# Performance work log

Hardware: AMD Instinct MI355X
Metric: run time of the kernel (lower is better)

Reference implementation:

```python
import jax, jax.numpy as jnp
import numpy as np

B, N, K = 32, 64, 128          # batch, atoms per cell, channel width (128x0e + 128x1o)
R_MAX = 5.0
NUM_BESSEL = 8
P_CUT = 5                       # num_polynomial_cutoff
AVG_NEIGH = 16.0                # avg_num_neighbors
H_MLP = 512                     # hidden_dimensions_size, n_hidden_dimensions = 2
FEAT = 5 * K                    # ((num_interactions-1)*4 + 1) * 128 = 640


def silu(x):
    return x * jax.nn.sigmoid(x)


def _bessel_cutoff(r, mask):
    # Bessel radial basis * polynomial cutoff (MACE), masked on valid edges.
    n = jnp.arange(1, NUM_BESSEL + 1, dtype=r.dtype)
    rb = jnp.sqrt(2.0 / R_MAX) * jnp.sin(n * (jnp.pi / R_MAX) * r[..., None]) / r[..., None]
    u = r / R_MAX
    p = float(P_CUT)
    fc = 1.0 - 0.5 * (p + 1) * (p + 2) * u**P_CUT + p * (p + 2) * u**(P_CUT + 1) - 0.5 * p * (p + 1) * u**(P_CUT + 2)
    fc = fc * (u < 1.0)
    return rb * (fc * mask)[..., None]


def _sph(uvec):
    # Real spherical harmonics l=0,1,2 (component normalization), uvec: unit edge vectors.
    x, y, z = uvec[..., 0], uvec[..., 1], uvec[..., 2]
    s3, s5, s15 = 3.0**0.5, 5.0**0.5, 15.0**0.5
    Y0 = jnp.ones_like(x)[..., None]
    Y1 = jnp.stack([s3 * x, s3 * y, s3 * z], -1)
    Y2 = jnp.stack([s15 * x * y, s15 * y * z, 0.5 * s5 * (3 * z * z - 1.0),
                    s15 * x * z, 0.5 * s15 * (x * x - y * y)], -1)
    return Y0, Y1, Y2


def _radial_mlp(x, w0, b0, w1, b1, w2, b2, w3, b3):
    h = silu(x @ w0 + b0)
    h = silu(h @ w1 + b1)
    h = silu(h @ w2 + b2)
    return h @ w3 + b3


def setup_inputs() -> dict:
    key = jax.random.key(0)
    ks = jax.random.split(key, 32)
    f32 = jnp.float32

    def lin(k, fan_in, shape):
        return (jax.random.normal(k, shape, dtype=f32) / np.sqrt(fan_in)).astype(f32)

    inp = {
        "noisy_relative_positions": jax.random.uniform(ks[0], (B, N, 3), dtype=f32),
        "time": jax.random.uniform(ks[1], (B, 1), dtype=f32),
        "unit_cell": (11.0 * jnp.eye(3, dtype=f32) + 0.3 * jax.random.uniform(ks[2], (B, 3, 3), dtype=f32)),
        "w_embed": lin(ks[3], 1, (K,)),
        # interaction 1 radial MLP: 8 -> 64 -> 64 -> 64 -> 3*K (weights for l=0,1,2 paths)
        "r1_w0": lin(ks[4], NUM_BESSEL, (NUM_BESSEL, 64)), "r1_b0": jnp.zeros((64,), f32),
        "r1_w1": lin(ks[5], 64, (64, 64)), "r1_b1": jnp.zeros((64,), f32),
        "r1_w2": lin(ks[6], 64, (64, 64)), "r1_b2": jnp.zeros((64,), f32),
        "r1_w3": lin(ks[7], 64, (64, 3 * K)), "r1_b3": jnp.zeros((3 * K,), f32),
        "mix1_l0": lin(ks[8], K, (K, K)),
        "mix1_l1": lin(ks[9], K, (K, K)),
        "mix1_l2": lin(ks[10], K, (K, K)),
        # interaction 2 radial MLP: 8 -> 64 -> 64 -> 64 -> 2*K (paths 0e x 0e -> 0e, 1o x 1o -> 0e)
        "r2_w0": lin(ks[11], NUM_BESSEL, (NUM_BESSEL, 64)), "r2_b0": jnp.zeros((64,), f32),
        "r2_w1": lin(ks[12], 64, (64, 64)), "r2_b1": jnp.zeros((64,), f32),
        "r2_w2": lin(ks[13], 64, (64, 64)), "r2_b2": jnp.zeros((64,), f32),
        "r2_w3": lin(ks[14], 64, (64, 2 * K)), "r2_b3": jnp.zeros((2 * K,), f32),
        "mix2": lin(ks[15], K, (K, K)),
        # readout MLP: 641 -> 512 -> 512 -> 3
        "mlp_w0": lin(ks[16], FEAT + 1, (FEAT + 1, H_MLP)), "mlp_b0": jnp.zeros((H_MLP,), f32),
        "mlp_w1": lin(ks[17], H_MLP, (H_MLP, H_MLP)), "mlp_b1": jnp.zeros((H_MLP,), f32),
        "mlp_w2": lin(ks[18], H_MLP, (H_MLP, 3)), "mlp_b2": jnp.zeros((3,), f32),
    }
    return inp


def reference(noisy_relative_positions, time, unit_cell, w_embed,
              r1_w0, r1_b0, r1_w1, r1_b1, r1_w2, r1_b2, r1_w3, r1_b3,
              mix1_l0, mix1_l1, mix1_l2,
              r2_w0, r2_b0, r2_w1, r2_b1, r2_w2, r2_b2, r2_w3, r2_b3, mix2,
              mlp_w0, mlp_b0, mlp_w1, mlp_b1, mlp_w2, mlp_b2):
    frac = noisy_relative_positions                      # [B,N,3] fractional
    d = frac[:, :, None, :] - frac[:, None, :, :]        # [B,N,N,3]
    d = d - jnp.round(d)                                 # minimum-image PBC
    dc = jnp.einsum('bijc,bcd->bijd', d, unit_cell)      # cartesian displacements
    r = jnp.sqrt(jnp.maximum(jnp.sum(dc * dc, -1), 1e-12))
    mask = (r < R_MAX) & (~jnp.eye(N, dtype=bool))[None]
    r_safe = jnp.where(mask, r, 1.0)
    uvec = dc / r_safe[..., None] * mask[..., None]      # unit edge vectors (0 off-edge)

    rad = _bessel_cutoff(r_safe, mask)                   # [B,N,N,8]
    Y0, Y1, Y2 = _sph(uvec)                              # [B,N,N,1|3|5]

    h0 = jnp.broadcast_to(w_embed, (B, N, K))            # element embedding (single species)

    # ---- interaction 1: radial-weighted tensor product h_j (x) Y_l, scatter over j ----
    we = _radial_mlp(rad, r1_w0, r1_b0, r1_w1, r1_b1, r1_w2, r1_b2, r1_w3, r1_b3)
    we = we.reshape(B, N, N, 3, K) * mask[..., None, None]
    hj = h0[:, None, :, :]                               # sender features [B,1,N,K]
    msg0 = jnp.einsum('bijk,bijm->bimk', we[..., 0, :] * hj, Y0)[:, :, 0] / AVG_NEIGH  # [B,N,K]
    msg1 = jnp.einsum('bijk,bijm->bimk', we[..., 1, :] * hj, Y1) / AVG_NEIGH           # [B,N,3,K]
    msg2 = jnp.einsum('bijk,bijm->bimk', we[..., 2, :] * hj, Y2) / AVG_NEIGH           # [B,N,5,K]

    s1 = msg0 @ mix1_l0 + jnp.sum(msg2 * msg2, axis=2) @ mix1_l2   # scalars [B,N,K]
    v1 = jnp.einsum('bimk,kc->bimc', msg1, mix1_l1)                # vectors [B,N,3,K]
    h1 = silu(s1)

    # ---- interaction 2: scalar output from 0e x 0e and 1o x 1o -> 0e paths ----
    we2 = _radial_mlp(rad, r2_w0, r2_b0, r2_w1, r2_b1, r2_w2, r2_b2, r2_w3, r2_b3)
    we2 = we2.reshape(B, N, N, 2, K) * mask[..., None, None]
    msg_a = jnp.sum(we2[..., 0, :] * h1[:, None, :, :], axis=2)    # [B,N,K]
    inv = jnp.einsum('bijm,bjmk->bijk', Y1, v1)                    # Y1 . v1_j invariant
    msg_b = jnp.sum(we2[..., 1, :] * inv, axis=2)
    s2 = ((msg_a + msg_b) / AVG_NEIGH) @ mix2                      # [B,N,K]

    # node_feats: layer1 full irreps (128x0e + 128x1o -> 512) + layer2 scalars (128) = 640
    node_feats = jnp.concatenate([s1, v1.reshape(B, N, 3 * K), s2], axis=-1)

    t = jnp.broadcast_to(time[:, None, :], (B, N, 1))
    x = jnp.concatenate([node_feats, t], axis=-1)                  # [B,N,641]
    x = jax.nn.relu(x @ mlp_w0 + mlp_b0)
    x = jax.nn.relu(x @ mlp_w1 + mlp_b1)
    return x @ mlp_w2 + mlp_b2                                     # [B,N,3]
```

## Files before the change

kernel.cpp:

```cpp
#include <hip/hip_runtime.h>
#include <math.h>

#define B_ 32
#define N_ 64
#define K_ 128
#define NPAIR (B_*N_*N_)

typedef __attribute__((ext_vector_type(8))) short short8;
typedef __attribute__((ext_vector_type(8))) __bf16 bf16x8;
typedef __attribute__((ext_vector_type(4))) float floatx4;

__device__ __forceinline__ float silu_f(float x) {
    return x / (1.0f + expf(-x));
}
__device__ __forceinline__ float4 ld4(const float* p) { return *(const float4*)p; }

__device__ __forceinline__ short f2bf(float x) {
    union { float f; unsigned u; } v; v.f = x;
    unsigned r = (v.u + 0x7FFFu + ((v.u >> 16) & 1u)) >> 16;
    return (short)r;
}
__device__ __forceinline__ float bf2f(short s) {
    union { unsigned u; float f; } v;
    v.u = ((unsigned)(unsigned short)s) << 16;
    return v.f;
}
__device__ __forceinline__ bf16x8 ld_frag(const short* p) {
    short8 r = *(const short8*)p;
    return __builtin_bit_cast(bf16x8, r);
}

__global__ __launch_bounds__(256) void prep_kernel(
    const float* __restrict__ r1w0, const float* __restrict__ r1w1,
    const float* __restrict__ r1w2, const float* __restrict__ r1w3,
    const float* __restrict__ r2w0, const float* __restrict__ r2w1,
    const float* __restrict__ r2w2, const float* __restrict__ r2w3,
    const float* __restrict__ mw0, const float* __restrict__ mw1,
    const float* __restrict__ wemb,
    const float* __restrict__ l0, const float* __restrict__ l1,
    const float* __restrict__ l2, short* __restrict__ dst)
{
    int idx = blockIdx.x * 256 + threadIdx.x;
    if (idx >= 733184) return;
    short v;
    if (idx < 4096) {
        int n = idx >> 6, k = idx & 63; v = f2bf(r1w1[k*64 + n]);
    } else if (idx < 8192) {
        int i = idx - 4096; int n = i >> 6, k = i & 63; v = f2bf(r1w2[k*64 + n]);
    } else if (idx < 12288) {
        int i = idx - 8192; int n = i >> 6, k = i & 63; v = f2bf(r2w1[k*64 + n]);
    } else if (idx < 16384) {
        int i = idx - 12288; int n = i >> 6, k = i & 63; v = f2bf(r2w2[k*64 + n]);
    } else if (idx < 32768) {
        int i = idx - 16384; int col = i >> 6, h = i & 63; v = f2bf(r2w3[h*256 + col]);
    } else if (idx < 393216) {
        int i = idx - 32768; int n = i / 704, k = i - n*704;
        v = (k < 641) ? f2bf(mw0[(size_t)k*512 + n]) : (short)0;
    } else if (idx < 655360) {
        int i = idx - 393216; int n = i >> 9, k = i & 511;
        v = f2bf(mw1[(size_t)k*512 + n]);
    } else if (idx < 657408) {
        int i = idx - 655360; int n = i >> 5, k = i & 31;
        v = (k < 8) ? f2bf(r1w0[k*64 + n]) : (short)0;
    } else if (idx < 659456) {
        int i = idx - 657408; int n = i >> 5, k = i & 31;
        v = (k < 8) ? f2bf(r2w0[k*64 + n]) : (short)0;
    } else if (idx < 684032) {
        int i = idx - 659456; int col = i >> 6, h = i & 63;
        v = f2bf(r1w3[h*384 + col] * wemb[col & 127] * 0.0625f);
    } else {
        int i = idx - 684032; int n = i / 384, k = i - n*384;
        float f;
        if (k < 128)       f = l0[k*128 + n];
        else if (k < 256)  f = l2[(k-128)*128 + n];
        else               f = l1[(k-256)*128 + n];
        v = f2bf(f);
    }
    dst[idx] = v;
}

__global__ __launch_bounds__(256) void geom_kernel(
    const float* __restrict__ pos, const float* __restrict__ cell,
    float* __restrict__ rad, float* __restrict__ Y1, float* __restrict__ Y2,
    float* __restrict__ maskf)
{
    int p = blockIdx.x * 256 + threadIdx.x;
    if (p >= NPAIR) return;
    int b = p >> 12;
    int ij = p & 4095;
    int i = ij >> 6, j = ij & 63;
    const float* pi = pos + (size_t)(b*N_ + i)*3;
    const float* pj = pos + (size_t)(b*N_ + j)*3;
    float d0 = pi[0]-pj[0], d1 = pi[1]-pj[1], d2 = pi[2]-pj[2];
    d0 -= rintf(d0); d1 -= rintf(d1); d2 -= rintf(d2);
    const float* C = cell + b*9;
    float dc0 = d0*C[0] + d1*C[3] + d2*C[6];
    float dc1 = d0*C[1] + d1*C[4] + d2*C[7];
    float dc2 = d0*C[2] + d1*C[5] + d2*C[8];
    float r2 = fmaxf(dc0*dc0 + dc1*dc1 + dc2*dc2, 1e-12f);
    float r = sqrtf(r2);
    bool m = (r < 5.0f) && (i != j);
    float mf = m ? 1.0f : 0.0f;
    float rs = m ? r : 1.0f;
    float inv_rs = 1.0f / rs;
    float x = dc0*inv_rs*mf, y = dc1*inv_rs*mf, z = dc2*inv_rs*mf;
    float u = r * 0.2f;
    float u2 = u*u, u4 = u2*u2, u5 = u4*u;
    float fc = 1.0f - 21.0f*u5 + 35.0f*u5*u - 15.0f*u5*u2;
    fc = (u < 1.0f) ? fc : 0.0f;
    float pref = 0.6324555320336759f * inv_rs * (fc * mf);
    float w = 0.6283185307179586f * rs;
    float sw = sinf(w), cw = cosf(w);
    float c2 = 2.0f * cw;
    float rr[8];
    float sp = 0.f, s = sw;
    #pragma unroll
    for (int n = 0; n < 8; n++) {
        rr[n] = pref * s;
        float ns = c2*s - sp;
        sp = s; s = ns;
    }
    float4 v0 = {rr[0], rr[1], rr[2], rr[3]};
    float4 v1 = {rr[4], rr[5], rr[6], rr[7]};
    *(float4*)&rad[(size_t)p*8]     = v0;
    *(float4*)&rad[(size_t)p*8 + 4] = v1;
    const float s3  = 1.7320508075688772f;
    const float s5  = 2.23606797749979f;
    const float s15 = 3.872983346207417f;
    float* y1 = Y1 + (size_t)p*3;
    y1[0] = s3*x; y1[1] = s3*y; y1[2] = s3*z;
    float* y2 = Y2 + (size_t)p*5;
    y2[0] = s15*x*y;
    y2[1] = s15*y*z;
    y2[2] = 0.5f*s5*(3.0f*z*z - 1.0f);
    y2[3] = s15*x*z;
    y2[4] = 0.5f*s15*(x*x - y*y);
    maskf[p] = mf;
}

template<bool TRANSPOSE_OUT>
__device__ __forceinline__ void mfma_layer_t(
    const short* __restrict__ src, const short* __restrict__ WT,
    const float* __restrict__ bias, short* __restrict__ dst,
    int wv, int qd, int nn)
{
    floatx4 acc[4];
    #pragma unroll
    for (int tt = 0; tt < 4; tt++) acc[tt] = (floatx4){0.f, 0.f, 0.f, 0.f};
    #pragma unroll
    for (int ks = 0; ks < 64; ks += 32) {
        bf16x8 a = ld_frag(&src[(wv*16 + nn)*72 + ks + qd*8]);
        #pragma unroll
        for (int tt = 0; tt < 4; tt++) {
            bf16x8 b = ld_frag(&WT[(tt*16 + nn)*64 + ks + qd*8]);
            acc[tt] = __builtin_amdgcn_mfma_f32_16x16x32_bf16(a, b, acc[tt], 0, 0, 0);
        }
    }
    #pragma unroll
    for (int tt = 0; tt < 4; tt++) {
        int col = tt*16 + nn;
        float bv = bias[col];
        #pragma unroll
        for (int i = 0; i < 4; i++) {
            int row = wv*16 + qd*4 + i;
            short val = f2bf(silu_f(acc[tt][i] + bv));
            if (TRANSPOSE_OUT) dst[col*72 + row] = val;
            else               dst[row*72 + col] = val;
        }
    }
}

__device__ __forceinline__ void mfma_layer0(
    const short* __restrict__ radB, const short* __restrict__ w0T,
    const float* __restrict__ bias, short* __restrict__ dst,
    int wv, int qd, int nn)
{
    bf16x8 a = ld_frag(&radB[(wv*16 + nn)*40 + qd*8]);
    #pragma unroll
    for (int tt = 0; tt < 4; tt++) {
        floatx4 acc = (floatx4){0.f, 0.f, 0.f, 0.f};
        bf16x8 b = ld_frag(&w0T[(tt*16 + nn)*32 + qd*8]);
        acc = __builtin_amdgcn_mfma_f32_16x16x32_bf16(a, b, acc, 0, 0, 0);
        int col = tt*16 + nn;
        float bv = bias[col];
        #pragma unroll
        for (int i = 0; i < 4; i++) {
            int row = wv*16 + qd*4 + i;
            dst[row*72 + col] = f2bf(silu_f(acc[i] + bv));
        }
    }
}

__global__ __launch_bounds__(256) void pass1_kernel(
    const float* __restrict__ rad, const float* __restrict__ Y1g,
    const float* __restrict__ Y2g, const float* __restrict__ maskg,
    const float* __restrict__ wemb,
    const short* __restrict__ w0T, const float* __restrict__ b0,
    const short* __restrict__ w1T, const float* __restrict__ b1,
    const short* __restrict__ w2T, const float* __restrict__ b2,
    const short* __restrict__ w3T, const float* __restrict__ b3,
    const short* __restrict__ lT, const float* __restrict__ timeg,
    float* __restrict__ h1g, float* __restrict__ v1g, short* __restrict__ featsb)
{
    __shared__ __align__(16) char pool[32832];
    short* radB = (short*)pool;
    short* hcT  = (short*)pool;
    short* actA = (short*)(pool + 9216);
    short* actB = (short*)(pool + 18432);
    short* A2   = (short*)(pool + 9216);
    float* msgF = (float*)(pool + 21760);
    short* YmB  = (short*)(pool + 27648);
    short* GB   = (short*)(pool + 29952);
    float* qF   = (float*)(pool + 32256);
    float* SY   = (float*)(pool + 32768);

    int t = threadIdx.x;
    int wv = t >> 6, lane = t & 63, qd = lane >> 4, nn = lane & 15;
    int node = blockIdx.x;
    int b = node >> 6;
    size_t pbase = (size_t)node * 64;

    for (int idx = t; idx < 2560; idx += 256) {
        int j = idx / 40, c = idx - j*40;
        radB[idx] = (c < 8) ? f2bf(rad[pbase*8 + j*8 + c]) : (short)0;
    }
    for (int idx = t; idx < 1152; idx += 256) YmB[idx] = 0;
    __syncthreads();

    if (t < 64) {
        int j = t;
        float mf = maskg[pbase + j];
        YmB[j] = f2bf(mf);
        #pragma unroll
        for (int m = 0; m < 3; m++) YmB[(1+m)*72 + j] = f2bf(Y1g[(pbase+j)*3 + m] * mf);
        #pragma unroll
        for (int m = 0; m < 5; m++) YmB[(4+m)*72 + j] = f2bf(Y2g[(pbase+j)*5 + m] * mf);
    }
    mfma_layer0(radB, w0T, b0, actA, wv, qd, nn);
    __syncthreads();

    mfma_layer_t<false>(actA, w1T, b1, actB, wv, qd, nn);
    __syncthreads();
    mfma_layer_t<true >(actB, w2T, b2, hcT,  wv, qd, nn);
    __syncthreads();

    if (t < 16) {
        float acc = 0.f;
        if (t < 9) for (int j = 0; j < 64; j++) acc += bf2f(YmB[t*72 + j]);
        SY[t] = acc;
    }
    {
        floatx4 accG = (floatx4){0.f, 0.f, 0.f, 0.f};
        #pragma unroll
        for (int ks = 0; ks < 64; ks += 32) {
            bf16x8 a = ld_frag(&YmB[nn*72 + ks + qd*8]);
            bf16x8 bfr = ld_frag(&hcT[(wv*16 + nn)*72 + ks + qd*8]);
            accG = __builtin_amdgcn_mfma_f32_16x16x32_bf16(a, bfr, accG, 0, 0, 0);
        }
        #pragma unroll
        for (int i = 0; i < 4; i++)
            GB[(qd*4 + i)*72 + wv*16 + nn] = f2bf(accG[i]);
    }
    __syncthreads();

    {
        bf16x8 a0f = ld_frag(&GB[nn*72 + 0  + qd*8]);
        bf16x8 a1f = ld_frag(&GB[nn*72 + 32 + qd*8]);
        #pragma unroll
        for (int tl = 0; tl < 6; tl++) {
            int col0 = (wv*6 + tl)*16;
            floatx4 acc = (floatx4){0.f, 0.f, 0.f, 0.f};
            bf16x8 b0f = ld_frag(&w3T[(col0 + nn)*64 + 0  + qd*8]);
            bf16x8 b1f = ld_frag(&w3T[(col0 + nn)*64 + 32 + qd*8]);
            acc = __builtin_amdgcn_mfma_f32_16x16x32_bf16(a0f, b0f, acc, 0, 0, 0);
            acc = __builtin_amdgcn_mfma_f32_16x16x32_bf16(a1f, b1f, acc, 0, 0, 0);
            int col = col0 + nn;
            int csec = col >> 7, k = col & 127;
            #pragma unroll
            for (int i = 0; i < 4; i++) {
                int m = qd*4 + i;
                bool valid = (csec == 0) ? (m == 0)
                           : (csec == 1) ? (m >= 1 && m <= 3)
                                         : (m >= 4 && m <= 8);
                if (valid)
                    msgF[m*128 + k] = acc[i] + SY[m]*b3[col]*wemb[k]*0.0625f;
            }
        }
    }
    __syncthreads();

    if (t < 128) {
        float acc = 0.f;
        #pragma unroll
        for (int m = 4; m < 9; m++) { float v = msgF[m*128 + t]; acc += v*v; }
        qF[t] = acc;
    }
    __syncthreads();

    for (int idx = t; idx < 6272; idx += 256) A2[idx] = 0;
    __syncthreads();
    {
        int idx = t;
        A2[idx] = (idx < 128) ? f2bf(msgF[idx]) : f2bf(qF[idx - 128]);
        if (t < 128) {
            #pragma unroll
            for (int m = 1; m <= 3; m++)
                A2[m*392 + 256 + t] = f2bf(msgF[m*128 + t]);
        }
    }
    __syncthreads();

    #pragma unroll
    for (int tt = 0; tt < 2; tt++) {
        int col = (wv*2 + tt)*16 + nn;
        floatx4 acc = (floatx4){0.f, 0.f, 0.f, 0.f};
        #pragma unroll
        for (int ks = 0; ks < 384; ks += 32) {
            bf16x8 a = ld_frag(&A2[nn*392 + ks + qd*8]);
            bf16x8 bfr = ld_frag(&lT[(size_t)col*384 + ks + qd*8]);
            acc = __builtin_amdgcn_mfma_f32_16x16x32_bf16(a, bfr, acc, 0, 0, 0);
        }
        if (qd == 0) {
            float s1 = acc[0];
            featsb[(size_t)node*704 + col] = f2bf(s1);
            h1g[(size_t)node*128 + col] = silu_f(s1);
            #pragma unroll
            for (int i = 1; i < 4; i++) {
                float v = acc[i];
                v1g[(size_t)node*384 + (i-1)*128 + col] = v;
                featsb[(size_t)node*704 + 128 + (i-1)*128 + col] = f2bf(v);
            }
        }
    }
    if (t == 0) featsb[(size_t)node*704 + 640] = f2bf(timeg[b]);
    if (t < 63) featsb[(size_t)node*704 + 641 + t] = 0;
}

__global__ __launch_bounds__(256) void pass2_kernel(
    const float* __restrict__ rad, const float* __restrict__ Y1g,
    const float* __restrict__ maskg,
    const short* __restrict__ w0T, const float* __restrict__ b0,
    const short* __restrict__ w1T, const float* __restrict__ b1,
    const short* __restrict__ w2T, const float* __restrict__ b2,
    const short* __restrict__ w3T, const float* __restrict__ b3,
    const float* __restrict__ mix2,
    const float* __restrict__ h1g, const float* __restrict__ v1g,
    short* __restrict__ featsb)
{
    __shared__ __align__(16) char pool[46848];
    short* radB  = (short*)pool;
    short* hc    = (short*)pool;
    short* actA  = (short*)(pool + 9216);
    short* actB  = (short*)(pool + 18432);
    short* h1B   = (short*)(pool + 9216);
    short* invB  = (short*)(pool + 27648);
    float* Y1s   = (float*)(pool + 45056);
    float* mask_s= (float*)(pool + 46080);
    float* msgab = (float*)(pool + 46336);

    int t = threadIdx.x;
    int wv = t >> 6, lane = t & 63, qd = lane >> 4, nn = lane & 15;
    int node = blockIdx.x;
    int b = node >> 6;
    size_t pbase = (size_t)node * 64;

    for (int idx = t; idx < 2560; idx += 256) {
        int j = idx / 40, c = idx - j*40;
        radB[idx] = (c < 8) ? f2bf(rad[pbase*8 + j*8 + c]) : (short)0;
    }
    if (t < 64) {
        mask_s[t] = maskg[pbase + t];
        #pragma unroll
        for (int m = 0; m < 3; m++) Y1s[t*4 + m] = Y1g[(pbase+t)*3 + m];
    }
    if (t < 128) msgab[t] = 0.f;
    __syncthreads();

    mfma_layer0(radB, w0T, b0, actA, wv, qd, nn);
    __syncthreads();
    mfma_layer_t<false>(actA, w1T, b1, actB, wv, qd, nn);
    __syncthreads();
    mfma_layer_t<false>(actB, w2T, b2, hc, wv, qd, nn);
    __syncthreads();

    for (int idx = t; idx < 2048; idx += 256) {
        int j = idx >> 5, kq = (idx & 31)*4;
        size_t gj = (size_t)b*64 + j;
        float4 hv = ld4(&h1g[gj*128 + kq]);
        h1B[j*136 + kq + 0] = f2bf(hv.x);
        h1B[j*136 + kq + 1] = f2bf(hv.y);
        h1B[j*136 + kq + 2] = f2bf(hv.z);
        h1B[j*136 + kq + 3] = f2bf(hv.w);
        const float* vb = &v1g[gj*384 + kq];
        float4 vx = ld4(vb), vy = ld4(vb + 128), vz = ld4(vb + 256);
        float yx = Y1s[j*4+0], yy = Y1s[j*4+1], yz = Y1s[j*4+2];
        invB[j*136 + kq + 0] = f2bf(yx*vx.x + yy*vy.x + yz*vz.x);
        invB[j*136 + kq + 1] = f2bf(yx*vx.y + yy*vy.y + yz*vz.y);
        invB[j*136 + kq + 2] = f2bf(yx*vx.z + yy*vy.z + yz*vz.z);
        invB[j*136 + kq + 3] = f2bf(yx*vx.w + yy*vy.w + yz*vz.w);
    }
    __syncthreads();

    {
        bf16x8 aA = ld_frag(&hc[(wv*16 + nn)*72 + 0  + qd*8]);
        bf16x8 aB = ld_frag(&hc[(wv*16 + nn)*72 + 32 + qd*8]);
        #pragma unroll
        for (int g = 0; g < 4; g++) {
            #pragma unroll
            for (int tt = 0; tt < 4; tt++) {
                int col0 = g*64 + tt*16;
                floatx4 acc = (floatx4){0.f, 0.f, 0.f, 0.f};
                bf16x8 b0f = ld_frag(&w3T[(col0 + nn)*64 + 0  + qd*8]);
                bf16x8 b1f = ld_frag(&w3T[(col0 + nn)*64 + 32 + qd*8]);
                acc = __builtin_amdgcn_mfma_f32_16x16x32_bf16(aA, b0f, acc, 0, 0, 0);
                acc = __builtin_amdgcn_mfma_f32_16x16x32_bf16(aB, b1f, acc, 0, 0, 0);
                int col = col0 + nn;
                int k = col & 127;
                float bias = b3[col];
                const short* src = (col < 128) ? h1B : invB;
                float p = 0.f;
                #pragma unroll
                for (int i = 0; i < 4; i++) {
                    int j = wv*16 + qd*4 + i;
                    float we = (acc[i] + bias) * mask_s[j];
                    p += we * bf2f(src[j*136 + k]);
                }
                p += __shfl_xor(p, 16);
                p += __shfl_xor(p, 32);
                if (qd == 0) atomicAdd(&msgab[k], p);
            }
        }
    }
    __syncthreads();

    if (t < 128) {
        float acc = 0.f;
        for (int k = 0; k < 128; k++) acc += msgab[k] * mix2[k*128 + t];
        featsb[(size_t)node*704 + 512 + t] = f2bf(acc * 0.0625f);
    }
}

__global__ __launch_bounds__(256) void gemm_mfma_kernel(
    const short* __restrict__ A, int lda,
    const short* __restrict__ BT, int ldb, int K,
    const float* __restrict__ bias, short* __restrict__ Cout, int ldo)
{
    __shared__ short As[64*72];
    __shared__ short Bs[64*72];
    int t = threadIdx.x;
    int wv = t >> 6, lane = t & 63, qd = lane >> 4, nn = lane & 15;
    int m0 = blockIdx.x * 64, n0 = blockIdx.y * 64;
    floatx4 acc[4];
    #pragma unroll
    for (int tt = 0; tt < 4; tt++) acc[tt] = (floatx4){0.f, 0.f, 0.f, 0.f};

    for (int kc = 0; kc < K; kc += 64) {
        for (int s = t; s < 512; s += 256) {
            int j = s >> 3, kk = (s & 7) * 8;
            *(uint4*)&As[j*72 + kk] = *(const uint4*)&A[(size_t)(m0 + j)*lda + kc + kk];
            *(uint4*)&Bs[j*72 + kk] = *(const uint4*)&BT[(size_t)(n0 + j)*ldb + kc + kk];
        }
        __syncthreads();
        #pragma unroll
        for (int ks = 0; ks < 64; ks += 32) {
            bf16x8 a = ld_frag(&As[(wv*16 + nn)*72 + ks + qd*8]);
            #pragma unroll
            for (int tt = 0; tt < 4; tt++) {
                bf16x8 bb = ld_frag(&Bs[(tt*16 + nn)*72 + ks + qd*8]);
                acc[tt] = __builtin_amdgcn_mfma_f32_16x16x32_bf16(a, bb, acc[tt], 0, 0, 0);
            }
        }
        __syncthreads();
    }
    #pragma unroll
    for (int tt = 0; tt < 4; tt++) {
        int n = n0 + tt*16 + nn;
        float bv = bias[n];
        #pragma unroll
        for (int i = 0; i < 4; i++) {
            int m = m0 + wv*16 + qd*4 + i;
            Cout[(size_t)m*ldo + n] = f2bf(fmaxf(acc[tt][i] + bv, 0.f));
        }
    }
}

__global__ __launch_bounds__(64) void final3_kernel(
    const short* __restrict__ H, const float* __restrict__ w2,
    const float* __restrict__ b2, float* __restrict__ out)
{
    int node = blockIdx.x, lane = threadIdx.x;
    float a0 = 0.f, a1 = 0.f, a2 = 0.f;
    #pragma unroll
    for (int r = 0; r < 8; r++) {
        int k = r*64 + lane;
        float h = bf2f(H[(size_t)node*512 + k]);
        a0 += h * w2[k*3 + 0];
        a1 += h * w2[k*3 + 1];
        a2 += h * w2[k*3 + 2];
    }
    #pragma unroll
    for (int off = 32; off > 0; off >>= 1) {
        a0 += __shfl_down(a0, off);
        a1 += __shfl_down(a1, off);
        a2 += __shfl_down(a2, off);
    }
    if (lane == 0) {
        out[(size_t)node*3 + 0] = a0 + b2[0];
        out[(size_t)node*3 + 1] = a1 + b2[1];
        out[(size_t)node*3 + 2] = a2 + b2[2];
    }
}

extern "C" void kernel_launch(void* const* d_in, const int* in_sizes, int n_in,
                              void* d_out, int out_size, void* d_ws, size_t ws_size,
                              hipStream_t stream) {
    const float* pos   = (const float*)d_in[0];
    const float* timeg = (const float*)d_in[1];
    const float* cell  = (const float*)d_in[2];
    const float* wemb  = (const float*)d_in[3];
    const float* r1w0  = (const float*)d_in[4];
    const float* r1b0  = (const float*)d_in[5];
    const float* r1w1  = (const float*)d_in[6];
    const float* r1b1  = (const float*)d_in[7];
    const float* r1w2  = (const float*)d_in[8];
    const float* r1b2  = (const float*)d_in[9];
    const float* r1w3  = (const float*)d_in[10];
    const float* r1b3  = (const float*)d_in[11];
    const float* l0    = (const float*)d_in[12];
    const float* l1    = (const float*)d_in[13];
    const float* l2    = (const float*)d_in[14];
    const float* r2w0  = (const float*)d_in[15];
    const float* r2b0  = (const float*)d_in[16];
    const float* r2w1  = (const float*)d_in[17];
    const float* r2b1  = (const float*)d_in[18];
    const float* r2w2  = (const float*)d_in[19];
    const float* r2b2  = (const float*)d_in[20];
    const float* r2w3  = (const float*)d_in[21];
    const float* r2b3  = (const float*)d_in[22];
    const float* mix2  = (const float*)d_in[23];
    const float* mw0   = (const float*)d_in[24];
    const float* mb0   = (const float*)d_in[25];
    const float* mw1   = (const float*)d_in[26];
    const float* mb1   = (const float*)d_in[27];
    const float* mw2   = (const float*)d_in[28];
    const float* mb2   = (const float*)d_in[29];

    float* ws    = (float*)d_ws;
    float* rad   = ws;
    float* Y1    = rad   + (size_t)NPAIR*8;
    float* Y2    = Y1    + (size_t)NPAIR*3;
    float* maskf = Y2    + (size_t)NPAIR*5;
    float* h1    = maskf + (size_t)NPAIR;
    float* v1    = h1    + (size_t)B_*N_*K_;
    short* featsb = (short*)(v1 + (size_t)B_*N_*3*K_);
    short* prep  = featsb + (size_t)2048*704;
    short* w1T_1 = prep;
    short* w2T_1 = prep + 4096;
    short* w1T_2 = prep + 8192;
    short* w2T_2 = prep + 12288;
    short* w3T_2 = prep + 16384;
    short* wT0   = prep + 32768;
    short* wT1   = prep + 393216;
    short* w0T_1 = prep + 655360;
    short* w0T_2 = prep + 657408;
    short* w3T_1 = prep + 659456;
    short* lT    = prep + 684032;
    short* h0bb = (short*)rad;
    short* h1bb = (short*)Y2;

    prep_kernel<<<(733184 + 255)/256, 256, 0, stream>>>(
        r1w0, r1w1, r1w2, r1w3, r2w0, r2w1, r2w2, r2w3, mw0, mw1,
        wemb, l0, l1, l2, prep);
    geom_kernel<<<NPAIR/256, 256, 0, stream>>>(pos, cell, rad, Y1, Y2, maskf);
    pass1_kernel<<<B_*N_, 256, 0, stream>>>(rad, Y1, Y2, maskf, wemb,
        w0T_1, r1b0, w1T_1, r1b1, w2T_1, r1b2, w3T_1, r1b3, lT, timeg,
        h1, v1, featsb);
    pass2_kernel<<<B_*N_, 256, 0, stream>>>(rad, Y1, maskf,
        w0T_2, r2b0, w1T_2, r2b1, w2T_2, r2b2, w3T_2, r2b3, mix2, h1, v1, featsb);
    dim3 g0(32, 8);
    gemm_mfma_kernel<<<g0, 256, 0, stream>>>(featsb, 704, wT0, 704, 704, mb0, h0bb, 512);
    gemm_mfma_kernel<<<g0, 256, 0, stream>>>(h0bb, 512, wT1, 512, 512, mb1, h1bb, 512);
    final3_kernel<<<B_*N_, 64, 0, stream>>>(h1bb, mw2, mb2, (float*)d_out);
}
```

Measured before the change: 292.2 us.

## Split radial MLPs into batched kernel, split-K head GEMMs, MFMA mix2 projection

The radial MLP hidden layers for both interactions move out of the per-node pass kernels into one bigmlp kernel that processes 128 edges per block and writes bf16 hidden activations to global memory. The message kernels then only run the final projection, and the r2 bias is folded into an extended weight. The radial basis and h1 are now stored as bf16. The mix2 projection moves from a scalar loop to a separate MFMA kernel. The head MLP GEMMs become split-K over 4 partitions with a combine kernel, which adds launches and extra global round trips of hidden and partial data in exchange for more parallelism.

```diff
diff --git a/kernel.cpp b/kernel.cpp
--- a/kernel.cpp
+++ b/kernel.cpp
@@ -35,13 +35,15 @@
     const float* __restrict__ r1w2, const float* __restrict__ r1w3,
     const float* __restrict__ r2w0, const float* __restrict__ r2w1,
     const float* __restrict__ r2w2, const float* __restrict__ r2w3,
+    const float* __restrict__ r2b3,
     const float* __restrict__ mw0, const float* __restrict__ mw1,
     const float* __restrict__ wemb,
     const float* __restrict__ l0, const float* __restrict__ l1,
-    const float* __restrict__ l2, short* __restrict__ dst)
+    const float* __restrict__ l2, const float* __restrict__ mix2,
+    short* __restrict__ dst)
 {
     int idx = blockIdx.x * 256 + threadIdx.x;
-    if (idx >= 733184) return;
+    if (idx >= 757760) return;
     short v;
     if (idx < 4096) {
         int n = idx >> 6, k = idx & 63; v = f2bf(r1w1[k*64 + n]);
@@ -51,37 +53,42 @@
         int i = idx - 8192; int n = i >> 6, k = i & 63; v = f2bf(r2w1[k*64 + n]);
     } else if (idx < 16384) {
         int i = idx - 12288; int n = i >> 6, k = i & 63; v = f2bf(r2w2[k*64 + n]);
-    } else if (idx < 32768) {
-        int i = idx - 16384; int col = i >> 6, h = i & 63; v = f2bf(r2w3[h*256 + col]);
-    } else if (idx < 393216) {
-        int i = idx - 32768; int n = i / 704, k = i - n*704;
+    } else if (idx < 40960) {
+        int i = idx - 16384; int col = i / 96, k = i - col*96;
+        v = (k < 64) ? f2bf(r2w3[k*256 + col])
+          : (k == 64) ? f2bf(r2b3[col]) : (short)0;
+    } else if (idx < 401408) {
+        int i = idx - 40960; int n = i / 704, k = i - n*704;
         v = (k < 641) ? f2bf(mw0[(size_t)k*512 + n]) : (short)0;
-    } else if (idx < 655360) {
-        int i = idx - 393216; int n = i >> 9, k = i & 511;
+    } else if (idx < 663552) {
+        int i = idx - 401408; int n = i >> 9, k = i & 511;
         v = f2bf(mw1[(size_t)k*512 + n]);
-    } else if (idx < 657408) {
-        int i = idx - 655360; int n = i >> 5, k = i & 31;
+    } else if (idx < 665600) {
+        int i = idx - 663552; int n = i >> 5, k = i & 31;
         v = (k < 8) ? f2bf(r1w0[k*64 + n]) : (short)0;
-    } else if (idx < 659456) {
-        int i = idx - 657408; int n = i >> 5, k = i & 31;
+    } else if (idx < 667648) {
+        int i = idx - 665600; int n = i >> 5, k = i & 31;
         v = (k < 8) ? f2bf(r2w0[k*64 + n]) : (short)0;
-    } else if (idx < 684032) {
-        int i = idx - 659456; int col = i >> 6, h = i & 63;
+    } else if (idx < 692224) {
+        int i = idx - 667648; int col = i >> 6, h = i & 63;
         v = f2bf(r1w3[h*384 + col] * wemb[col & 127] * 0.0625f);
-    } else {
-        int i = idx - 684032; int n = i / 384, k = i - n*384;
+    } else if (idx < 741376) {
+        int i = idx - 692224; int n = i / 384, k = i - n*384;
         float f;
         if (k < 128)       f = l0[k*128 + n];
         else if (k < 256)  f = l2[(k-128)*128 + n];
         else               f = l1[(k-256)*128 + n];
         v = f2bf(f);
+    } else {
+        int i = idx - 741376; int n = i >> 7, k = i & 127;
+        v = f2bf(mix2[k*128 + n] * 0.0625f);
     }
     dst[idx] = v;
 }
 
 __global__ __launch_bounds__(256) void geom_kernel(
     const float* __restrict__ pos, const float* __restrict__ cell,
-    float* __restrict__ rad, float* __restrict__ Y1, float* __restrict__ Y2,
+    short* __restrict__ radbf, float* __restrict__ Y1, float* __restrict__ Y2,
     float* __restrict__ maskf)
 {
     int p = blockIdx.x * 256 + threadIdx.x;
@@ -112,18 +119,15 @@
     float w = 0.6283185307179586f * rs;
     float sw = sinf(w), cw = cosf(w);
     float c2 = 2.0f * cw;
-    float rr[8];
+    short8 sv;
     float sp = 0.f, s = sw;
     #pragma unroll
     for (int n = 0; n < 8; n++) {
-        rr[n] = pref * s;
+        sv[n] = f2bf(pref * s);
         float ns = c2*s - sp;
         sp = s; s = ns;
     }
-    float4 v0 = {rr[0], rr[1], rr[2], rr[3]};
-    float4 v1 = {rr[4], rr[5], rr[6], rr[7]};
-    *(float4*)&rad[(size_t)p*8]     = v0;
-    *(float4*)&rad[(size_t)p*8 + 4] = v1;
+    *(short8*)&radbf[(size_t)p*8] = sv;
     const float s3  = 1.7320508075688772f;
     const float s5  = 2.23606797749979f;
     const float s15 = 3.872983346207417f;
@@ -138,81 +142,126 @@
     maskf[p] = mf;
 }
 
-template<bool TRANSPOSE_OUT>
-__device__ __forceinline__ void mfma_layer_t(
-    const short* __restrict__ src, const short* __restrict__ WT,
-    const float* __restrict__ bias, short* __restrict__ dst,
-    int wv, int qd, int nn)
-{
-    floatx4 acc[4];
-    #pragma unroll
-    for (int tt = 0; tt < 4; tt++) acc[tt] = (floatx4){0.f, 0.f, 0.f, 0.f};
-    #pragma unroll
-    for (int ks = 0; ks < 64; ks += 32) {
-        bf16x8 a = ld_frag(&src[(wv*16 + nn)*72 + ks + qd*8]);
-        #pragma unroll
-        for (int tt = 0; tt < 4; tt++) {
-            bf16x8 b = ld_frag(&WT[(tt*16 + nn)*64 + ks + qd*8]);
-            acc[tt] = __builtin_amdgcn_mfma_f32_16x16x32_bf16(a, b, acc[tt], 0, 0, 0);
-        }
-    }
-    #pragma unroll
-    for (int tt = 0; tt < 4; tt++) {
-        int col = tt*16 + nn;
-        float bv = bias[col];
-        #pragma unroll
-        for (int i = 0; i < 4; i++) {
-            int row = wv*16 + qd*4 + i;
-            short val = f2bf(silu_f(acc[tt][i] + bv));
-            if (TRANSPOSE_OUT) dst[col*72 + row] = val;
-            else               dst[row*72 + col] = val;
-        }
-    }
-}
-
-__device__ __forceinline__ void mfma_layer0(
-    const short* __restrict__ radB, const short* __restrict__ w0T,
-    const float* __restrict__ bias, short* __restrict__ dst,
-    int wv, int qd, int nn)
-{
-    bf16x8 a = ld_frag(&radB[(wv*16 + nn)*40 + qd*8]);
-    #pragma unroll
-    for (int tt = 0; tt < 4; tt++) {
-        floatx4 acc = (floatx4){0.f, 0.f, 0.f, 0.f};
-        bf16x8 b = ld_frag(&w0T[(tt*16 + nn)*32 + qd*8]);
-        acc = __builtin_amdgcn_mfma_f32_16x16x32_bf16(a, b, acc, 0, 0, 0);
-        int col = tt*16 + nn;
-        float bv = bias[col];
-        #pragma unroll
-        for (int i = 0; i < 4; i++) {
-            int row = wv*16 + qd*4 + i;
-            dst[row*72 + col] = f2bf(silu_f(acc[i] + bv));
-        }
-    }
-}
-
-__global__ __launch_bounds__(256) void pass1_kernel(
-    const float* __restrict__ rad, const float* __restrict__ Y1g,
+__global__ __launch_bounds__(256) void bigmlp_kernel(
+    const short* __restrict__ radbf,
+    const short* __restrict__ w0T1, const float* __restrict__ b01,
+    const short* __restrict__ w1T1, const float* __restrict__ b11,
+    const short* __restrict__ w2T1, const float* __restrict__ b21,
+    short* __restrict__ hc1,
+    const short* __restrict__ w0T2, const float* __restrict__ b02,
+    const short* __restrict__ w1T2, const float* __restrict__ b12,
+    const short* __restrict__ w2T2, const float* __restrict__ b22,
+    short* __restrict__ hc2)
+{
+    __shared__ short radB[128*40];
+    __shared__ short actA[128*72];
+    __shared__ short actB[128*72];
+    int t = threadIdx.x;
+    int wv = t >> 6, lane = t & 63, qd = lane >> 4, nn = lane & 15;
+    size_t p0 = (size_t)blockIdx.x * 128;
+
+    if (t < 128) {
+        uint4 rv = *(const uint4*)&radbf[(p0 + t)*8];
+        uint4 z = {0,0,0,0};
+        *(uint4*)&radB[t*40]      = rv;
+        *(uint4*)&radB[t*40 + 8]  = z;
+        *(uint4*)&radB[t*40 + 16] = z;
+        *(uint4*)&radB[t*40 + 24] = z;
+        *(uint4*)&radB[t*40 + 32] = z;
+    }
+    __syncthreads();
+
+    const short* w0Ts[2] = {w0T1, w0T2};
+    const short* w1Ts[2] = {w1T1, w1T2};
+    const short* w2Ts[2] = {w2T1, w2T2};
+    const float* b0s[2]  = {b01, b02};
+    const float* b1s[2]  = {b11, b12};
+    const float* b2s[2]  = {b21, b22};
+    short* hcs[2] = {hc1, hc2};
+
+    for (int net = 0; net < 2; net++) {
+        const short* w0T = w0Ts[net];
+        const short* w1T = w1Ts[net];
+        const short* w2T = w2Ts[net];
+        const float* b0 = b0s[net];
+        const float* b1 = b1s[net];
+        const float* b2 = b2s[net];
+        short* hc = hcs[net];
+        #pragma unroll
+        for (int ms = 0; ms < 2; ms++) {
+            int r0 = wv*32 + ms*16;
+            bf16x8 a = ld_frag(&radB[(r0 + nn)*40 + qd*8]);
+            #pragma unroll
+            for (int tt = 0; tt < 4; tt++) {
+                floatx4 acc = (floatx4){0.f,0.f,0.f,0.f};
+                bf16x8 bb = ld_frag(&w0T[(tt*16 + nn)*32 + qd*8]);
+                acc = __builtin_amdgcn_mfma_f32_16x16x32_bf16(a, bb, acc, 0, 0, 0);
+                int col = tt*16 + nn;
+                float bv = b0[col];
+                #pragma unroll
+                for (int i = 0; i < 4; i++)
+                    actA[(r0 + qd*4 + i)*72 + col] = f2bf(silu_f(acc[i] + bv));
+            }
+        }
+        __syncthreads();
+        #pragma unroll
+        for (int ms = 0; ms < 2; ms++) {
+            int r0 = wv*32 + ms*16;
+            bf16x8 a0 = ld_frag(&actA[(r0 + nn)*72 + qd*8]);
+            bf16x8 a1 = ld_frag(&actA[(r0 + nn)*72 + 32 + qd*8]);
+            #pragma unroll
+            for (int tt = 0; tt < 4; tt++) {
+                floatx4 acc = (floatx4){0.f,0.f,0.f,0.f};
+                bf16x8 b0f = ld_frag(&w1T[(tt*16 + nn)*64 + qd*8]);
+                bf16x8 b1f = ld_frag(&w1T[(tt*16 + nn)*64 + 32 + qd*8]);
+                acc = __builtin_amdgcn_mfma_f32_16x16x32_bf16(a0, b0f, acc, 0, 0, 0);
+                acc = __builtin_amdgcn_mfma_f32_16x16x32_bf16(a1, b1f, acc, 0, 0, 0);
+                int col = tt*16 + nn;
+                float bv = b1[col];
+                #pragma unroll
+                for (int i = 0; i < 4; i++)
+                    actB[(r0 + qd*4 + i)*72 + col] = f2bf(silu_f(acc[i] + bv));
+            }
+        }
+        __syncthreads();
+        #pragma unroll
+        for (int ms = 0; ms < 2; ms++) {
+            int r0 = wv*32 + ms*16;
+            bf16x8 a0 = ld_frag(&actB[(r0 + nn)*72 + qd*8]);
+            bf16x8 a1 = ld_frag(&actB[(r0 + nn)*72 + 32 + qd*8]);
+            #pragma unroll
+            for (int tt = 0; tt < 4; tt++) {
+                floatx4 acc = (floatx4){0.f,0.f,0.f,0.f};
+                bf16x8 b0f = ld_frag(&w2T[(tt*16 + nn)*64 + qd*8]);
+                bf16x8 b1f = ld_frag(&w2T[(tt*16 + nn)*64 + 32 + qd*8]);
+                acc = __builtin_amdgcn_mfma_f32_16x16x32_bf16(a0, b0f, acc, 0, 0, 0);
+                acc = __builtin_amdgcn_mfma_f32_16x16x32_bf16(a1, b1f, acc, 0, 0, 0);
+                int col = tt*16 + nn;
+                float bv = b2[col];
+                #pragma unroll
+                for (int i = 0; i < 4; i++)
+                    hc[(p0 + r0 + qd*4 + i)*64 + col] = f2bf(silu_f(acc[i] + bv));
+            }
+        }
+    }
+}
+
+__global__ __launch_bounds__(256) void msg1_kernel(
+    const short* __restrict__ hc1, const float* __restrict__ Y1g,
     const float* __restrict__ Y2g, const float* __restrict__ maskg,
-    const float* __restrict__ wemb,
-    const short* __restrict__ w0T, const float* __restrict__ b0,
-    const short* __restrict__ w1T, const float* __restrict__ b1,
-    const short* __restrict__ w2T, const float* __restrict__ b2,
-    const short* __restrict__ w3T, const float* __restrict__ b3,
-    const short* __restrict__ lT, const float* __restrict__ timeg,
-    float* __restrict__ h1g, float* __restrict__ v1g, short* __restrict__ featsb)
-{
-    __shared__ __align__(16) char pool[32832];
-    short* radB = (short*)pool;
+    const float* __restrict__ wemb, const float* __restrict__ b3,
+    const short* __restrict__ w3T, const short* __restrict__ lT,
+    const float* __restrict__ timeg,
+    short* __restrict__ h1bf, float* __restrict__ v1g, short* __restrict__ featsb)
+{
+    __shared__ __align__(16) char pool[19008];
     short* hcT  = (short*)pool;
-    short* actA = (short*)(pool + 9216);
-    short* actB = (short*)(pool + 18432);
-    short* A2   = (short*)(pool + 9216);
-    float* msgF = (float*)(pool + 21760);
-    short* YmB  = (short*)(pool + 27648);
-    short* GB   = (short*)(pool + 29952);
-    float* qF   = (float*)(pool + 32256);
-    float* SY   = (float*)(pool + 32768);
+    short* A2   = (short*)pool;
+    short* YmB  = (short*)(pool + 9216);
+    short* GB   = (short*)(pool + 11520);
+    float* msgF = (float*)(pool + 13824);
+    float* qF   = (float*)(pool + 18432);
+    float* SY   = (float*)(pool + 18944);
 
     int t = threadIdx.x;
     int wv = t >> 6, lane = t & 63, qd = lane >> 4, nn = lane & 15;
@@ -220,13 +269,14 @@
     int b = node >> 6;
     size_t pbase = (size_t)node * 64;
 
-    for (int idx = t; idx < 2560; idx += 256) {
-        int j = idx / 40, c = idx - j*40;
-        radB[idx] = (c < 8) ? f2bf(rad[pbase*8 + j*8 + c]) : (short)0;
+    for (int idx = t; idx < 512; idx += 256) {
+        int j = idx >> 3, h0 = (idx & 7)*8;
+        short8 v = *(const short8*)&hc1[((size_t)node*64 + j)*64 + h0];
+        #pragma unroll
+        for (int q = 0; q < 8; q++) hcT[(h0 + q)*72 + j] = v[q];
     }
     for (int idx = t; idx < 1152; idx += 256) YmB[idx] = 0;
     __syncthreads();
-
     if (t < 64) {
         int j = t;
         float mf = maskg[pbase + j];
@@ -236,21 +286,14 @@
         #pragma unroll
         for (int m = 0; m < 5; m++) YmB[(4+m)*72 + j] = f2bf(Y2g[(pbase+j)*5 + m] * mf);
     }
-    mfma_layer0(radB, w0T, b0, actA, wv, qd, nn);
-    __syncthreads();
-
-    mfma_layer_t<false>(actA, w1T, b1, actB, wv, qd, nn);
-    __syncthreads();
-    mfma_layer_t<true >(actB, w2T, b2, hcT,  wv, qd, nn);
-    __syncthreads();
-
+    __syncthreads();
     if (t < 16) {
         float acc = 0.f;
         if (t < 9) for (int j = 0; j < 64; j++) acc += bf2f(YmB[t*72 + j]);
         SY[t] = acc;
     }
     {
-        floatx4 accG = (floatx4){0.f, 0.f, 0.f, 0.f};
+        floatx4 accG = (floatx4){0.f,0.f,0.f,0.f};
         #pragma unroll
         for (int ks = 0; ks < 64; ks += 32) {
             bf16x8 a = ld_frag(&YmB[nn*72 + ks + qd*8]);
@@ -262,14 +305,13 @@
             GB[(qd*4 + i)*72 + wv*16 + nn] = f2bf(accG[i]);
     }
     __syncthreads();
-
     {
         bf16x8 a0f = ld_frag(&GB[nn*72 + 0  + qd*8]);
         bf16x8 a1f = ld_frag(&GB[nn*72 + 32 + qd*8]);
         #pragma unroll
         for (int tl = 0; tl < 6; tl++) {
             int col0 = (wv*6 + tl)*16;
-            floatx4 acc = (floatx4){0.f, 0.f, 0.f, 0.f};
+            floatx4 acc = (floatx4){0.f,0.f,0.f,0.f};
             bf16x8 b0f = ld_frag(&w3T[(col0 + nn)*64 + 0  + qd*8]);
             bf16x8 b1f = ld_frag(&w3T[(col0 + nn)*64 + 32 + qd*8]);
             acc = __builtin_amdgcn_mfma_f32_16x16x32_bf16(a0f, b0f, acc, 0, 0, 0);
@@ -288,7 +330,6 @@
         }
     }
     __syncthreads();
-
     if (t < 128) {
         float acc = 0.f;
         #pragma unroll
@@ -296,24 +337,19 @@
         qF[t] = acc;
     }
     __syncthreads();
-
     for (int idx = t; idx < 6272; idx += 256) A2[idx] = 0;
     __syncthreads();
-    {
-        int idx = t;
-        A2[idx] = (idx < 128) ? f2bf(msgF[idx]) : f2bf(qF[idx - 128]);
-        if (t < 128) {
-            #pragma unroll
-            for (int m = 1; m <= 3; m++)
-                A2[m*392 + 256 + t] = f2bf(msgF[m*128 + t]);
-        }
-    }
-    __syncthreads();
-
+    A2[t] = (t < 128) ? f2bf(msgF[t]) : f2bf(qF[t - 128]);
+    if (t < 128) {
+        #pragma unroll
+        for (int m = 1; m <= 3; m++)
+            A2[m*392 + 256 + t] = f2bf(msgF[m*128 + t]);
+    }
+    __syncthreads();
     #pragma unroll
     for (int tt = 0; tt < 2; tt++) {
         int col = (wv*2 + tt)*16 + nn;
-        floatx4 acc = (floatx4){0.f, 0.f, 0.f, 0.f};
+        floatx4 acc = (floatx4){0.f,0.f,0.f,0.f};
         #pragma unroll
         for (int ks = 0; ks < 384; ks += 32) {
             bf16x8 a = ld_frag(&A2[nn*392 + ks + qd*8]);
@@ -323,7 +359,7 @@
         if (qd == 0) {
             float s1 = acc[0];
             featsb[(size_t)node*704 + col] = f2bf(s1);
-            h1g[(size_t)node*128 + col] = silu_f(s1);
+            h1bf[(size_t)node*128 + col] = f2bf(silu_f(s1));
             #pragma unroll
             for (int i = 1; i < 4; i++) {
                 float v = acc[i];
@@ -336,27 +372,18 @@
     if (t < 63) featsb[(size_t)node*704 + 641 + t] = 0;
 }
 
-__global__ __launch_bounds__(256) void pass2_kernel(
-    const float* __restrict__ rad, const float* __restrict__ Y1g,
-    const float* __restrict__ maskg,
-    const short* __restrict__ w0T, const float* __restrict__ b0,
-    const short* __restrict__ w1T, const float* __restrict__ b1,
-    const short* __restrict__ w2T, const float* __restrict__ b2,
-    const short* __restrict__ w3T, const float* __restrict__ b3,
-    const float* __restrict__ mix2,
-    const float* __restrict__ h1g, const float* __restrict__ v1g,
-    short* __restrict__ featsb)
-{
-    __shared__ __align__(16) char pool[46848];
-    short* radB  = (short*)pool;
-    short* hc    = (short*)pool;
-    short* actA  = (short*)(pool + 9216);
-    short* actB  = (short*)(pool + 18432);
-    short* h1B   = (short*)(pool + 9216);
-    short* invB  = (short*)(pool + 27648);
-    float* Y1s   = (float*)(pool + 45056);
-    float* mask_s= (float*)(pool + 46080);
-    float* msgab = (float*)(pool + 46336);
+__global__ __launch_bounds__(256) void msg2_kernel(
+    const short* __restrict__ hc2, const float* __restrict__ Y1g,
+    const float* __restrict__ maskg, const short* __restrict__ w3extT,
+    const short* __restrict__ h1bf, const float* __restrict__ v1g,
+    short* __restrict__ msgabf)
+{
+    __shared__ __align__(16) char pool[50688];
+    short* hc2e  = (short*)pool;
+    short* h1B   = (short*)(pool + 14336);
+    short* invB  = (short*)(pool + 31744);
+    float* Y1s   = (float*)(pool + 49152);
+    float* msgab = (float*)(pool + 50176);
 
     int t = threadIdx.x;
     int wv = t >> 6, lane = t & 63, qd = lane >> 4, nn = lane & 15;
@@ -364,34 +391,36 @@
     int b = node >> 6;
     size_t pbase = (size_t)node * 64;
 
-    for (int idx = t; idx < 2560; idx += 256) {
-        int j = idx / 40, c = idx - j*40;
-        radB[idx] = (c < 8) ? f2bf(rad[pbase*8 + j*8 + c]) : (short)0;
-    }
     if (t < 64) {
-        mask_s[t] = maskg[pbase + t];
-        #pragma unroll
-        for (int m = 0; m < 3; m++) Y1s[t*4 + m] = Y1g[(pbase+t)*3 + m];
+        int j = t;
+        #pragma unroll
+        for (int m = 0; m < 3; m++) Y1s[j*4 + m] = Y1g[(pbase+j)*3 + m];
+        float mf = maskg[pbase + j];
+        short8 z8 = {0,0,0,0,0,0,0,0};
+        *(short8*)&hc2e[j*112 + 64] = z8;
+        *(short8*)&hc2e[j*112 + 72] = z8;
+        *(short8*)&hc2e[j*112 + 80] = z8;
+        *(short8*)&hc2e[j*112 + 88] = z8;
+        *(short8*)&hc2e[j*112 + 96] = z8;
+        *(short8*)&hc2e[j*112 + 104] = z8;
+        hc2e[j*112 + 64] = f2bf(mf);
+    }
+    for (int idx = t; idx < 512; idx += 256) {
+        int j = idx >> 3, h0 = (idx & 7)*8;
+        short8 v = *(const short8*)&hc2[((size_t)node*64 + j)*64 + h0];
+        float mf = maskg[pbase + j];
+        if (mf == 0.f) { short8 z8 = {0,0,0,0,0,0,0,0}; v = z8; }
+        *(short8*)&hc2e[j*112 + h0] = v;
+    }
+    for (int idx = t; idx < 1024; idx += 256) {
+        int j = idx >> 4, k0 = (idx & 15)*8;
+        *(uint4*)&h1B[j*136 + k0] = *(const uint4*)&h1bf[((size_t)b*64 + j)*128 + k0];
     }
     if (t < 128) msgab[t] = 0.f;
     __syncthreads();
-
-    mfma_layer0(radB, w0T, b0, actA, wv, qd, nn);
-    __syncthreads();
-    mfma_layer_t<false>(actA, w1T, b1, actB, wv, qd, nn);
-    __syncthreads();
-    mfma_layer_t<false>(actB, w2T, b2, hc, wv, qd, nn);
-    __syncthreads();
-
     for (int idx = t; idx < 2048; idx += 256) {
         int j = idx >> 5, kq = (idx & 31)*4;
-        size_t gj = (size_t)b*64 + j;
-        float4 hv = ld4(&h1g[gj*128 + kq]);
-        h1B[j*136 + kq + 0] = f2bf(hv.x);
-        h1B[j*136 + kq + 1] = f2bf(hv.y);
-        h1B[j*136 + kq + 2] = f2bf(hv.z);
-        h1B[j*136 + kq + 3] = f2bf(hv.w);
-        const float* vb = &v1g[gj*384 + kq];
+        const float* vb = &v1g[((size_t)b*64 + j)*384 + kq];
         float4 vx = ld4(vb), vy = ld4(vb + 128), vz = ld4(vb + 256);
         float yx = Y1s[j*4+0], yy = Y1s[j*4+1], yz = Y1s[j*4+2];
         invB[j*136 + kq + 0] = f2bf(yx*vx.x + yy*vy.x + yz*vz.x);
@@ -400,30 +429,29 @@
         invB[j*136 + kq + 3] = f2bf(yx*vx.w + yy*vy.w + yz*vz.w);
     }
     __syncthreads();
-
     {
-        bf16x8 aA = ld_frag(&hc[(wv*16 + nn)*72 + 0  + qd*8]);
-        bf16x8 aB = ld_frag(&hc[(wv*16 + nn)*72 + 32 + qd*8]);
-        #pragma unroll
+        bf16x8 a0 = ld_frag(&hc2e[(wv*16 + nn)*112 + 0  + qd*8]);
+        bf16x8 a1 = ld_frag(&hc2e[(wv*16 + nn)*112 + 32 + qd*8]);
+        bf16x8 a2 = ld_frag(&hc2e[(wv*16 + nn)*112 + 64 + qd*8]);
         for (int g = 0; g < 4; g++) {
             #pragma unroll
             for (int tt = 0; tt < 4; tt++) {
                 int col0 = g*64 + tt*16;
-                floatx4 acc = (floatx4){0.f, 0.f, 0.f, 0.f};
-                bf16x8 b0f = ld_frag(&w3T[(col0 + nn)*64 + 0  + qd*8]);
-                bf16x8 b1f = ld_frag(&w3T[(col0 + nn)*64 + 32 + qd*8]);
-                acc = __builtin_amdgcn_mfma_f32_16x16x32_bf16(aA, b0f, acc, 0, 0, 0);
-                acc = __builtin_amdgcn_mfma_f32_16x16x32_bf16(aB, b1f, acc, 0, 0, 0);
+                floatx4 acc = (floatx4){0.f,0.f,0.f,0.f};
+                bf16x8 b0f = ld_frag(&w3extT[(col0 + nn)*96 + 0  + qd*8]);
+                bf16x8 b1f = ld_frag(&w3extT[(col0 + nn)*96 + 32 + qd*8]);
+                bf16x8 b2f = ld_frag(&w3extT[(col0 + nn)*96 + 64 + qd*8]);
+                acc = __builtin_amdgcn_mfma_f32_16x16x32_bf16(a0, b0f, acc, 0, 0, 0);
+                acc = __builtin_amdgcn_mfma_f32_16x16x32_bf16(a1, b1f, acc, 0, 0, 0);
+                acc = __builtin_amdgcn_mfma_f32_16x16x32_bf16(a2, b2f, acc, 0, 0, 0);
                 int col = col0 + nn;
                 int k = col & 127;
-                float bias = b3[col];
                 const short* src = (col < 128) ? h1B : invB;
                 float p = 0.f;
                 #pragma unroll
                 for (int i = 0; i < 4; i++) {
                     int j = wv*16 + qd*4 + i;
-                    float we = (acc[i] + bias) * mask_s[j];
-                    p += we * bf2f(src[j*136 + k]);
+                    p += acc[i] * bf2f(src[j*136 + k]);
                 }
                 p += __shfl_xor(p, 16);
                 p += __shfl_xor(p, 32);
@@ -432,56 +460,89 @@
         }
     }
     __syncthreads();
-
-    if (t < 128) {
-        float acc = 0.f;
-        for (int k = 0; k < 128; k++) acc += msgab[k] * mix2[k*128 + t];
-        featsb[(size_t)node*704 + 512 + t] = f2bf(acc * 0.0625f);
-    }
-}
-
-__global__ __launch_bounds__(256) void gemm_mfma_kernel(
+    if (t < 128) msgabf[(size_t)node*128 + t] = f2bf(msgab[t]);
+}
+
+__global__ __launch_bounds__(64) void s2_kernel(
+    const short* __restrict__ msgabf, const short* __restrict__ mix2T,
+    short* __restrict__ featsb)
+{
+    int lane = threadIdx.x, qd = lane >> 4, nn = lane & 15;
+    int m0 = blockIdx.x * 16, n0 = blockIdx.y * 64;
+    floatx4 acc[4];
+    #pragma unroll
+    for (int tt = 0; tt < 4; tt++) acc[tt] = (floatx4){0.f,0.f,0.f,0.f};
+    #pragma unroll
+    for (int ks = 0; ks < 128; ks += 32) {
+        bf16x8 a = ld_frag(&msgabf[(size_t)(m0 + nn)*128 + ks + qd*8]);
+        #pragma unroll
+        for (int tt = 0; tt < 4; tt++) {
+            bf16x8 bb = ld_frag(&mix2T[(size_t)(n0 + tt*16 + nn)*128 + ks + qd*8]);
+            acc[tt] = __builtin_amdgcn_mfma_f32_16x16x32_bf16(a, bb, acc[tt], 0, 0, 0);
+        }
+    }
+    #pragma unroll
+    for (int tt = 0; tt < 4; tt++) {
+        int n = n0 + tt*16 + nn;
+        #pragma unroll
+        for (int i = 0; i < 4; i++) {
+            int m = m0 + qd*4 + i;
+            featsb[(size_t)m*704 + 512 + n] = f2bf(acc[tt][i]);
+        }
+    }
+}
+
+__global__ __launch_bounds__(256) void gemm_part_kernel(
     const short* __restrict__ A, int lda,
-    const short* __restrict__ BT, int ldb, int K,
-    const float* __restrict__ bias, short* __restrict__ Cout, int ldo)
-{
-    __shared__ short As[64*72];
-    __shared__ short Bs[64*72];
+    const short* __restrict__ BT, int ldb,
+    int ngran, int nsplit, float* __restrict__ Cp)
+{
     int t = threadIdx.x;
     int wv = t >> 6, lane = t & 63, qd = lane >> 4, nn = lane & 15;
-    int m0 = blockIdx.x * 64, n0 = blockIdx.y * 64;
+    int m0 = blockIdx.x * 64, n0 = blockIdx.y * 64, z = blockIdx.z;
+    int g0 = (z*ngran)/nsplit, g1 = ((z+1)*ngran)/nsplit;
     floatx4 acc[4];
     #pragma unroll
-    for (int tt = 0; tt < 4; tt++) acc[tt] = (floatx4){0.f, 0.f, 0.f, 0.f};
-
-    for (int kc = 0; kc < K; kc += 64) {
-        for (int s = t; s < 512; s += 256) {
-            int j = s >> 3, kk = (s & 7) * 8;
-            *(uint4*)&As[j*72 + kk] = *(const uint4*)&A[(size_t)(m0 + j)*lda + kc + kk];
-            *(uint4*)&Bs[j*72 + kk] = *(const uint4*)&BT[(size_t)(n0 + j)*ldb + kc + kk];
-        }
-        __syncthreads();
-        #pragma unroll
-        for (int ks = 0; ks < 64; ks += 32) {
-            bf16x8 a = ld_frag(&As[(wv*16 + nn)*72 + ks + qd*8]);
-            #pragma unroll
-            for (int tt = 0; tt < 4; tt++) {
-                bf16x8 bb = ld_frag(&Bs[(tt*16 + nn)*72 + ks + qd*8]);
-                acc[tt] = __builtin_amdgcn_mfma_f32_16x16x32_bf16(a, bb, acc[tt], 0, 0, 0);
-            }
-        }
-        __syncthreads();
-    }
+    for (int tt = 0; tt < 4; tt++) acc[tt] = (floatx4){0.f,0.f,0.f,0.f};
+    int row = wv*16 + nn;
+    for (int g = g0; g < g1; g++) {
+        int k = g*32;
+        bf16x8 a = ld_frag(&A[(size_t)(m0 + row)*lda + k + qd*8]);
+        #pragma unroll
+        for (int tt = 0; tt < 4; tt++) {
+            bf16x8 bb = ld_frag(&BT[(size_t)(n0 + tt*16 + nn)*ldb + k + qd*8]);
+            acc[tt] = __builtin_amdgcn_mfma_f32_16x16x32_bf16(a, bb, acc[tt], 0, 0, 0);
+        }
+    }
+    float* out = Cp + (size_t)z*2048*512;
     #pragma unroll
     for (int tt = 0; tt < 4; tt++) {
         int n = n0 + tt*16 + nn;
-        float bv = bias[n];
-        #pragma unroll
-        for (int i = 0; i < 4; i++) {
-            int m = m0 + wv*16 + qd*4 + i;
-            Cout[(size_t)m*ldo + n] = f2bf(fmaxf(acc[tt][i] + bv, 0.f));
-        }
-    }
+        #pragma unroll
+        for (int i = 0; i < 4; i++)
+            out[(size_t)(m0 + wv*16 + qd*4 + i)*512 + n] = acc[tt][i];
+    }
+}
+
+__global__ __launch_bounds__(256) void combine_kernel(
+    const float* __restrict__ Cp, const float* __restrict__ bias,
+    short* __restrict__ out)
+{
+    int idx = (blockIdx.x * 256 + threadIdx.x) * 4;
+    int n = idx & 511;
+    float4 s = ld4(&Cp[idx]);
+    #pragma unroll
+    for (int z = 1; z < 4; z++) {
+        float4 p = ld4(&Cp[(size_t)z*1048576 + idx]);
+        s.x += p.x; s.y += p.y; s.z += p.z; s.w += p.w;
+    }
+    float4 bv = ld4(&bias[n]);
+    short4 o;
+    o.x = f2bf(fmaxf(s.x + bv.x, 0.f));
+    o.y = f2bf(fmaxf(s.y + bv.y, 0.f));
+    o.z = f2bf(fmaxf(s.z + bv.z, 0.f));
+    o.w = f2bf(fmaxf(s.w + bv.w, 0.f));
+    *(short4*)&out[idx] = o;
 }
 
 __global__ __launch_bounds__(64) void final3_kernel(
@@ -545,40 +606,57 @@
     const float* mw2   = (const float*)d_in[28];
     const float* mb2   = (const float*)d_in[29];
 
-    float* ws    = (float*)d_ws;
-    float* rad   = ws;
-    float* Y1    = rad   + (size_t)NPAIR*8;
-    float* Y2    = Y1    + (size_t)NPAIR*3;
-    float* maskf = Y2    + (size_t)NPAIR*5;
-    float* h1    = maskf + (size_t)NPAIR;
-    float* v1    = h1    + (size_t)B_*N_*K_;
-    short* featsb = (short*)(v1 + (size_t)B_*N_*3*K_);
-    short* prep  = featsb + (size_t)2048*704;
-    short* w1T_1 = prep;
-    short* w2T_1 = prep + 4096;
-    short* w1T_2 = prep + 8192;
-    short* w2T_2 = prep + 12288;
-    short* w3T_2 = prep + 16384;
-    short* wT0   = prep + 32768;
-    short* wT1   = prep + 393216;
-    short* w0T_1 = prep + 655360;
-    short* w0T_2 = prep + 657408;
-    short* w3T_1 = prep + 659456;
-    short* lT    = prep + 684032;
-    short* h0bb = (short*)rad;
+    float* ws = (float*)d_ws;
+    short* radbf  = (short*)ws;
+    float* Y1     = ws + 524288;
+    float* Y2     = ws + 917504;
+    float* maskf  = ws + 1572864;
+    float* v1     = ws + 1703936;
+    short* featsb = (short*)(ws + 2490368);
+    short* prep   = (short*)(ws + 3211264);
+    short* hc1    = (short*)(ws + 3590144);
+    short* hc2    = (short*)(ws + 7784448);
+    short* h1bf   = (short*)(ws + 11978752);
+    short* msgabf = (short*)(ws + 12109824);
+
+    short* w1T_1  = prep;
+    short* w2T_1  = prep + 4096;
+    short* w1T_2  = prep + 8192;
+    short* w2T_2  = prep + 12288;
+    short* w3extT = prep + 16384;
+    short* wT0    = prep + 40960;
+    short* wT1    = prep + 401408;
+    short* w0T_1  = prep + 663552;
+    short* w0T_2  = prep + 665600;
+    short* w3T_1  = prep + 667648;
+    short* lT     = prep + 692224;
+    short* mix2T  = prep + 741376;
+
+    float* Cp   = (float*)hc1;
+    short* h0bb = radbf;
     short* h1bb = (short*)Y2;
 
-    prep_kernel<<<(733184 + 255)/256, 256, 0, stream>>>(
-        r1w0, r1w1, r1w2, r1w3, r2w0, r2w1, r2w2, r2w3, mw0, mw1,
-        wemb, l0, l1, l2, prep);
-    geom_kernel<<<NPAIR/256, 256, 0, stream>>>(pos, cell, rad, Y1, Y2, maskf);
-    pass1_kernel<<<B_*N_, 256, 0, stream>>>(rad, Y1, Y2, maskf, wemb,
-        w0T_1, r1b0, w1T_1, r1b1, w2T_1, r1b2, w3T_1, r1b3, lT, timeg,
-        h1, v1, featsb);
-    pass2_kernel<<<B_*N_, 256, 0, stream>>>(rad, Y1, maskf,
-        w0T_2, r2b0, w1T_2, r2b1, w2T_2, r2b2, w3T_2, r2b3, mix2, h1, v1, featsb);
-    dim3 g0(32, 8);
-    gemm_mfma_kernel<<<g0, 256, 0, stream>>>(featsb, 704, wT0, 704, 704, mb0, h0bb, 512);
-    gemm_mfma_kernel<<<g0, 256, 0, stream>>>(h0bb, 512, wT1, 512, 512, mb1, h1bb, 512);
+    prep_kernel<<<(757760 + 255)/256, 256, 0, stream>>>(
+        r1w0, r1w1, r1w2, r1w3, r2w0, r2w1, r2w2, r2w3, r2b3,
+        mw0, mw1, wemb, l0, l1, l2, mix2, prep);
+    geom_kernel<<<NPAIR/256, 256, 0, stream>>>(pos, cell, radbf, Y1, Y2, maskf);
+    bigmlp_kernel<<<NPAIR/128, 256, 0, stream>>>(radbf,
+        w0T_1, r1b0, w1T_1, r1b1, w2T_1, r1b2, hc1,
+        w0T_2, r2b0, w1T_2, r2b1, w2T_2, r2b2, hc2);
+    msg1_kernel<<<B_*N_, 256, 0, stream>>>(hc1, Y1, Y2, maskf, wemb, r1b3,
+        w3T_1, lT, timeg, h1bf, v1, featsb);
+    msg2_kernel<<<B_*N_, 256, 0, stream>>>(hc2, Y1, maskf, w3extT, h1bf, v1,
+        msgabf);
+    {
+        dim3 g(128, 2);
+        s2_kernel<<<g, 64, 0, stream>>>(msgabf, mix2T, featsb);
+    }
+    {
+        dim3 g(32, 8, 4);
+        gemm_part_kernel<<<g, 256, 0, stream>>>(featsb, 704, wT0, 704, 22, 4, Cp);
+        combine_kernel<<<1024, 256, 0, stream>>>(Cp, mb0, h0bb);
+        gemm_part_kernel<<<g, 256, 0, stream>>>(h0bb, 512, wT1, 512, 16, 4, Cp);
+        combine_kernel<<<1024, 256, 0, stream>>>(Cp, mb1, h1bb);
+    }
     final3_kernel<<<B_*N_, 64, 0, stream>>>(h1bb, mw2, mb2, (float*)d_out);
 }
```

Result: slower. 322.0 us (+10.2%).
